# Optimization experiments

Measured on AMD Instinct MI355X. Metric: run time of the kernel, lower is better.

Reference implementation:

```python
import jax, jax.numpy as jnp
import numpy as np


def setup_inputs() -> dict:
    key = jax.random.key(0)
    ks = jax.random.split(key, 6)
    bs, n_src, n_tgt = 4, 4096, 16384
    c_src, c_tgt = 256, 128
    xyz_target = jax.random.uniform(ks[0], (bs, n_tgt, 3), dtype=jnp.float32)
    xyz_source = jax.random.uniform(ks[1], (bs, n_src, 3), dtype=jnp.float32)
    feats_target = jax.random.normal(ks[2], (bs, n_tgt, c_tgt), dtype=jnp.float32)
    feats_source = jax.random.normal(ks[3], (bs, n_src, c_src), dtype=jnp.float32)
    # SharedMlP 1x1 conv weights (1,1,cin,cout) squeezed to (cin,cout)
    w1 = jax.random.normal(ks[4], (c_src + c_tgt, 256), dtype=jnp.float32) * (1.0 / np.sqrt(c_src + c_tgt))
    w2 = jax.random.normal(ks[5], (256, 256), dtype=jnp.float32) * (1.0 / np.sqrt(256))
    return {"xyz_target": xyz_target, "xyz_source": xyz_source,
            "feats_target": feats_target, "feats_source": feats_source,
            "w1": w1, "w2": w2}


def reference(xyz_target, xyz_source, feats_target, feats_source, w1, w2):
    # --- three_nn: full pairwise euclidean distance [bs, n_tgt, n_src] ---
    diff = xyz_target[:, :, None, :] - xyz_source[:, None, :, :]
    dis = jnp.linalg.norm(diff, axis=-1)                      # bs, n_tgt, n_src
    neg_dis, idx = jax.lax.top_k(-dis, 3)                     # 3 nearest
    nn_dis = jnp.maximum(-neg_dis, 1e-10)                     # bs, n_tgt, 3
    inv = 1.0 / nn_dis
    weight = inv / jnp.sum(inv, axis=-1, keepdims=True)       # bs, n_tgt, 3
    # --- three_interpolate: batched gather + weighted reduce ---
    feats_sel = jax.vmap(lambda f, i: f[i])(feats_source, idx)  # bs, n_tgt, 3, c
    w_sum = jnp.sum(weight, axis=-1, keepdims=True) + 1e-6
    interp = jnp.einsum('btk,btkc->btc', weight, feats_sel) / w_sum
    # --- concat skip features, 1x1-conv MLP (pointwise matmul) ---
    x = jnp.concatenate([interp, feats_target], axis=2)       # bs, n_tgt, 384
    x = jax.nn.relu(jnp.einsum('btc,cd->btd', x, w1))
    x = jax.nn.relu(jnp.einsum('btc,cd->btd', x, w2))
    return x
```

## Files before the change

### kernel.cpp

```cpp
#include <hip/hip_runtime.h>
#include <hip/hip_bf16.h>
#include <stdint.h>

#define BS 4
#define NS 4096
#define NT 16384
#define CS 256
#define CT 128
#define NOUT 256
#define MTOT (BS*NT)
#define GR 8
#define NC (GR*GR*GR)
#define HCELL 0.125f

typedef __attribute__((ext_vector_type(4))) float floatx4;
typedef __attribute__((ext_vector_type(8))) short shortx8;
typedef __attribute__((ext_vector_type(8))) unsigned short ushortx8;
typedef __attribute__((ext_vector_type(8))) __bf16 bf16x8;

__device__ __forceinline__ unsigned short f2bf(float f) {
  unsigned int u = __builtin_bit_cast(unsigned int, f);
  u += 0x7FFFu + ((u >> 16) & 1u);
  return (unsigned short)(u >> 16);
}
__device__ __forceinline__ float bf2f(unsigned short u) {
  return __builtin_bit_cast(float, ((unsigned int)u) << 16);
}
__device__ __forceinline__ int cell_of(float x) {
  int c = (int)(x * 8.0f);
  return min(7, max(0, c));
}

__global__ __launch_bounds__(256) void wt_kernel(const float* __restrict__ w1,
    const float* __restrict__ w2, unsigned short* __restrict__ w1at,
    unsigned short* __restrict__ w1bt, unsigned short* __restrict__ w2t) {
  int i = blockIdx.x * 256 + threadIdx.x;
  {
    int n = i >> 8, k = i & 255;
    w1at[i] = f2bf(w1[k * NOUT + n]);
    w2t[i]  = f2bf(w2[k * NOUT + n]);
  }
  if (i < 256 * 128) {
    int n = i >> 7, k = i & 127;
    w1bt[i] = f2bf(w1[(256 + k) * NOUT + n]);
  }
}

__global__ __launch_bounds__(512) void bucket_src(const float* __restrict__ xyzs,
    float4* __restrict__ bsrc, int* __restrict__ soff) {
  __shared__ int cnt[NC];
  __shared__ int scan[NC];
  int tid = threadIdx.x;
  int b = blockIdx.x;
  const float* src = xyzs + (size_t)b * NS * 3;
  cnt[tid] = 0;
  __syncthreads();
  #pragma unroll
  for (int k = 0; k < 8; ++k) {
    int p = k * 512 + tid;
    float x = src[3*p], y = src[3*p+1], z = src[3*p+2];
    int c = (cell_of(z) * GR + cell_of(y)) * GR + cell_of(x);
    atomicAdd(&cnt[c], 1);
  }
  __syncthreads();
  scan[tid] = cnt[tid];
  __syncthreads();
  for (int off = 1; off < NC; off <<= 1) {
    int v = (tid >= off) ? scan[tid - off] : 0;
    __syncthreads();
    scan[tid] += v;
    __syncthreads();
  }
  int excl = scan[tid] - cnt[tid];
  cnt[tid] = excl;
  soff[b * (NC + 1) + tid] = excl;
  if (tid == 0) soff[b * (NC + 1) + NC] = NS;
  __syncthreads();
  #pragma unroll
  for (int k = 0; k < 8; ++k) {
    int p = k * 512 + tid;
    float x = src[3*p], y = src[3*p+1], z = src[3*p+2];
    int c = (cell_of(z) * GR + cell_of(y)) * GR + cell_of(x);
    int slot = atomicAdd(&cnt[c], 1);
    bsrc[(size_t)b * NS + slot] = make_float4(x, y, z, __int_as_float(p));
  }
}

__global__ __launch_bounds__(1024) void sort_tgt(const float* __restrict__ xyzt,
    float4* __restrict__ stgt) {
  __shared__ int cnt[NC];
  __shared__ int scan[NC];
  int tid = threadIdx.x;
  int b = blockIdx.x;
  const float* tp = xyzt + (size_t)b * NT * 3;
  if (tid < NC) cnt[tid] = 0;
  __syncthreads();
  #pragma unroll
  for (int k = 0; k < 16; ++k) {
    int p = k * 1024 + tid;
    float x = tp[3*p], y = tp[3*p+1], z = tp[3*p+2];
    int c = (cell_of(z) * GR + cell_of(y)) * GR + cell_of(x);
    atomicAdd(&cnt[c], 1);
  }
  __syncthreads();
  if (tid < NC) scan[tid] = cnt[tid];
  __syncthreads();
  for (int off = 1; off < NC; off <<= 1) {
    int v = (tid < NC && tid >= off) ? scan[tid - off] : 0;
    __syncthreads();
    if (tid < NC) scan[tid] += v;
    __syncthreads();
  }
  if (tid < NC) cnt[tid] = scan[tid] - cnt[tid];
  __syncthreads();
  #pragma unroll
  for (int k = 0; k < 16; ++k) {
    int p = k * 1024 + tid;
    float x = tp[3*p], y = tp[3*p+1], z = tp[3*p+2];
    int c = (cell_of(z) * GR + cell_of(y)) * GR + cell_of(x);
    int slot = atomicAdd(&cnt[c], 1);
    stgt[(size_t)b * NT + slot] = make_float4(x, y, z, __int_as_float(p));
  }
}

__device__ __forceinline__ void ins3(float sc, int jj,
    float& d0, float& d1, float& d2, int& i0, int& i1, int& i2) {
  bool l0 = sc < d0, l1 = sc < d1, l2 = sc < d2;
  d2 = l1 ? d1 : (l2 ? sc : d2);
  i2 = l1 ? i1 : (l2 ? jj : i2);
  d1 = l0 ? d0 : (l1 ? sc : d1);
  i1 = l0 ? i0 : (l1 ? jj : i1);
  d0 = l0 ? sc : d0;
  i0 = l0 ? jj : i0;
}

__device__ __forceinline__ void pair_merge(float& d0, float& d1, float& d2,
                                           int& i0, int& i1, int& i2,
                                           int delta, int sub) {
  float e0 = __shfl_xor(d0, delta);
  float e1 = __shfl_xor(d1, delta);
  float e2 = __shfl_xor(d2, delta);
  int   y0 = __shfl_xor(i0, delta);
  int   y1 = __shfl_xor(i1, delta);
  int   y2 = __shfl_xor(i2, delta);
  float a0,a1,a2,b0,b1,b2; int x0,x1,x2,z0,z1,z2;
  if ((sub & delta) == 0) { a0=d0;a1=d1;a2=d2; x0=i0;x1=i1;x2=i2;
                            b0=e0;b1=e1;b2=e2; z0=y0;z1=y1;z2=y2; }
  else                    { a0=e0;a1=e1;a2=e2; x0=y0;x1=y1;x2=y2;
                            b0=d0;b1=d1;b2=d2; z0=i0;z1=i1;z2=i2; }
  bool t = a0 <= b0;
  d0 = t ? a0 : b0; i0 = t ? x0 : z0;
  float na0 = t ? a1 : a0; int nx0 = t ? x1 : x0;
  float na1 = t ? a2 : a1; int nx1 = t ? x2 : x1;
  float nb0 = t ? b0 : b1; int nz0 = t ? z0 : z1;
  float nb1 = t ? b1 : b2; int nz1 = t ? z1 : z2;
  t = na0 <= nb0;
  d1 = t ? na0 : nb0; i1 = t ? nx0 : nz0;
  float ma0 = t ? na1 : na0; int mx0 = t ? nx1 : nx0;
  float mb0 = t ? nb0 : nb1; int mz0 = t ? nz0 : nz1;
  t = ma0 <= mb0;
  d2 = t ? ma0 : mb0; i2 = t ? mx0 : mz0;
}

__global__ __launch_bounds__(256) void nn_kernel(const float4* __restrict__ stgt,
    const float4* __restrict__ bsrc, const int* __restrict__ soff,
    int* __restrict__ idx_out, float* __restrict__ w_out) {
  __shared__ float4 s_src[NS];
  __shared__ int s_off[NC + 1];
  int tid = threadIdx.x;
  int b = blockIdx.x >> 7;
  int tseg = blockIdx.x & 127;
  for (int i = tid; i < NS; i += 256) s_src[i] = bsrc[(size_t)b * NS + i];
  for (int i = tid; i < NC + 1; i += 256) s_off[i] = soff[b * (NC + 1) + i];
  __syncthreads();
  int tpair = tid >> 1, half = tid & 1;
  float4 tg = stgt[(size_t)b * NT + tseg * 128 + tpair];
  float tx = tg.x, ty = tg.y, tz = tg.z;
  int orig = __float_as_int(tg.w);
  int cx = cell_of(tx), cy = cell_of(ty), cz = cell_of(tz);
  int wx = min(max(cx, 1), 6) - 1;
  int wy = min(max(cy, 1), 6) - 1;
  int wz = min(max(cz, 1), 6) - 1;
  float d0 = 1e30f, d1 = 1e30f, d2 = 1e30f;
  int i0 = 0, i1 = 0, i2 = 0;
  for (int r = half; r < 9; r += 2) {
    int ez = wz + r / 3, ey = wy + r % 3;
    int rowc = (ez * GR + ey) * GR + wx;
    int lo = s_off[rowc], hi = s_off[rowc + 3];
    for (int p = lo; p < hi; ++p) {
      float4 s = s_src[p];
      float dx = tx - s.x, dy = ty - s.y, dz = tz - s.z;
      float q = dx*dx + dy*dy + dz*dz;
      ins3(q, __float_as_int(s.w), d0, d1, d2, i0, i1, i2);
    }
  }
  pair_merge(d0, d1, d2, i0, i1, i2, 1, half);
  float clx = fminf(wx > 0 ? tx - wx * HCELL : 1e30f,
                    wx + 3 < GR ? (wx + 3) * HCELL - tx : 1e30f);
  float cly = fminf(wy > 0 ? ty - wy * HCELL : 1e30f,
                    wy + 3 < GR ? (wy + 3) * HCELL - ty : 1e30f);
  float clz = fminf(wz > 0 ? tz - wz * HCELL : 1e30f,
                    wz + 3 < GR ? (wz + 3) * HCELL - tz : 1e30f);
  float cl = fminf(clx, fminf(cly, clz));
  bool bad = d2 > cl * cl;
  if (__any(bad)) {
    if (bad) {
      d0 = d1 = d2 = 1e30f; i0 = i1 = i2 = 0;
      for (int p = half; p < NS; p += 2) {
        float4 s = s_src[p];
        float dx = tx - s.x, dy = ty - s.y, dz = tz - s.z;
        float q = dx*dx + dy*dy + dz*dz;
        ins3(q, __float_as_int(s.w), d0, d1, d2, i0, i1, i2);
      }
    }
    pair_merge(d0, d1, d2, i0, i1, i2, 1, half);
  }
  if (half == 0) {
    float r0 = fmaxf(sqrtf(d0), 1e-10f);
    float r1 = fmaxf(sqrtf(d1), 1e-10f);
    float r2 = fmaxf(sqrtf(d2), 1e-10f);
    float v0 = 1.f/r0, v1 = 1.f/r1, v2 = 1.f/r2;
    float sc = 1.f / ((v0 + v1 + v2) * (1.f + 1e-6f));
    size_t o = ((size_t)b * NT + orig) * 3;
    idx_out[o] = i0; idx_out[o+1] = i1; idx_out[o+2] = i2;
    w_out[o] = v0*sc; w_out[o+1] = v1*sc; w_out[o+2] = v2*sc;
  }
}

__global__ __launch_bounds__(256) void gemm_g(const float* __restrict__ fs,
    const unsigned short* __restrict__ w1at, unsigned short* __restrict__ G) {
  constexpr int LDT = 72;
  __shared__ __attribute__((aligned(16))) unsigned short sA[128 * LDT];
  __shared__ __attribute__((aligned(16))) unsigned short sB[128 * LDT];
  int tid = threadIdx.x;
  int m0 = blockIdx.x * 128;
  int n0 = blockIdx.y * 128;
  int wave = tid >> 6, lane = tid & 63;
  int wm = (wave >> 1) * 64, wn = (wave & 1) * 64;
  int fr = lane & 15, quad = lane >> 4;
  floatx4 zero = {0.f, 0.f, 0.f, 0.f};
  floatx4 acc[4][4];
  #pragma unroll
  for (int i = 0; i < 4; ++i)
    #pragma unroll
    for (int j = 0; j < 4; ++j) acc[i][j] = zero;

  for (int kt = 0; kt < 256; kt += 64) {
    #pragma unroll
    for (int i = 0; i < 4; ++i) {
      int u = tid + 256 * i;
      int r = u >> 3, k8 = (u & 7) * 8;
      const float* src = fs + (size_t)(m0 + r) * 256 + kt + k8;
      float4 f0 = *(const float4*)src;
      float4 f1 = *(const float4*)(src + 4);
      ushortx8 o;
      o[0]=f2bf(f0.x); o[1]=f2bf(f0.y); o[2]=f2bf(f0.z); o[3]=f2bf(f0.w);
      o[4]=f2bf(f1.x); o[5]=f2bf(f1.y); o[6]=f2bf(f1.z); o[7]=f2bf(f1.w);
      *(ushortx8*)&sA[r * LDT + k8] = o;
    }
    #pragma unroll
    for (int i = 0; i < 4; ++i) {
      int u = tid + 256 * i;
      int n = u >> 3, kc = (u & 7) * 8;
      *(ushortx8*)&sB[n * LDT + kc] =
          *(const ushortx8*)(w1at + (size_t)(n0 + n) * 256 + kt + kc);
    }
    __syncthreads();
    #pragma unroll
    for (int kk = 0; kk < 64; kk += 32) {
      bf16x8 af[4], bfr[4];
      #pragma unroll
      for (int mi = 0; mi < 4; ++mi)
        af[mi] = __builtin_bit_cast(bf16x8,
            *(const ushortx8*)&sA[(wm + mi*16 + fr)*LDT + kk + quad*8]);
      #pragma unroll
      for (int ni = 0; ni < 4; ++ni)
        bfr[ni] = __builtin_bit_cast(bf16x8,
            *(const ushortx8*)&sB[(wn + ni*16 + fr)*LDT + kk + quad*8]);
      #pragma unroll
      for (int mi = 0; mi < 4; ++mi)
        #pragma unroll
        for (int ni = 0; ni < 4; ++ni)
          acc[mi][ni] = __builtin_amdgcn_mfma_f32_16x16x32_bf16(
              af[mi], bfr[ni], acc[mi][ni], 0, 0, 0);
    }
    __syncthreads();
  }
  #pragma unroll
  for (int mi = 0; mi < 4; ++mi)
    #pragma unroll
    for (int ni = 0; ni < 4; ++ni)
      #pragma unroll
      for (int r = 0; r < 4; ++r) {
        int grow = m0 + wm + mi*16 + quad*4 + r;
        int gcol = n0 + wn + ni*16 + fr;
        G[(size_t)grow * 256 + gcol] = f2bf(acc[mi][ni][r]);
      }
}

__global__ __launch_bounds__(256) void fused_mlp(const float* __restrict__ ft,
    const unsigned short* __restrict__ G, const int* __restrict__ idxb,
    const float* __restrict__ wgtb, const unsigned short* __restrict__ w1bt,
    const unsigned short* __restrict__ w2t, float* __restrict__ out) {
  constexpr int LDI = 264;
  constexpr int LDT = 72;
  __shared__ __attribute__((aligned(16))) unsigned short sI[64 * LDI];
  __shared__ __attribute__((aligned(16))) unsigned short sA[64 * LDT];
  __shared__ __attribute__((aligned(16))) unsigned short sB[256 * LDT];
  int tid = threadIdx.x;
  int row0 = blockIdx.x * 64;
  int b = row0 >> 14;
  int wave = tid >> 6, lane = tid & 63;
  int wn = wave * 64;
  int fr = lane & 15, quad = lane >> 4;

  {
    int r = tid >> 2, seg = tid & 3;
    int grow = row0 + r;
    const int* ip = idxb + (size_t)grow * 3;
    const float* wp = wgtb + (size_t)grow * 3;
    int g0i = ip[0], g1i = ip[1], g2i = ip[2];
    float w0 = wp[0], w1v = wp[1], w2v = wp[2];
    const unsigned short* Gb = G + ((size_t)b << 20);
    const unsigned short* g0 = Gb + ((size_t)g0i << 8) + seg * 64;
    const unsigned short* g1 = Gb + ((size_t)g1i << 8) + seg * 64;
    const unsigned short* g2 = Gb + ((size_t)g2i << 8) + seg * 64;
    #pragma unroll
    for (int j = 0; j < 8; ++j) {
      ushortx8 a = *(const ushortx8*)(g0 + j*8);
      ushortx8 c = *(const ushortx8*)(g1 + j*8);
      ushortx8 e = *(const ushortx8*)(g2 + j*8);
      ushortx8 o;
      #pragma unroll
      for (int q = 0; q < 8; ++q)
        o[q] = f2bf(w0*bf2f(a[q]) + w1v*bf2f(c[q]) + w2v*bf2f(e[q]));
      *(ushortx8*)&sI[r * LDI + seg * 64 + j * 8] = o;
    }
  }

  floatx4 zero = {0.f, 0.f, 0.f, 0.f};
  floatx4 acc[4][4];
  #pragma unroll
  for (int i = 0; i < 4; ++i)
    #pragma unroll
    for (int j = 0; j < 4; ++j) acc[i][j] = zero;

  for (int kt = 0; kt < 128; kt += 64) {
    #pragma unroll
    for (int i = 0; i < 2; ++i) {
      int u = tid + 256 * i;
      int r = u >> 3, k8 = (u & 7) * 8;
      const float* src = ft + (size_t)(row0 + r) * CT + kt + k8;
      float4 f0 = *(const float4*)src;
      float4 f1 = *(const float4*)(src + 4);
      ushortx8 o;
      o[0]=f2bf(f0.x); o[1]=f2bf(f0.y); o[2]=f2bf(f0.z); o[3]=f2bf(f0.w);
      o[4]=f2bf(f1.x); o[5]=f2bf(f1.y); o[6]=f2bf(f1.z); o[7]=f2bf(f1.w);
      *(ushortx8*)&sA[r * LDT + k8] = o;
    }
    #pragma unroll
    for (int i = 0; i < 8; ++i) {
      int u = tid + 256 * i;
      int n = u >> 3, kc = (u & 7) * 8;
      *(ushortx8*)&sB[n * LDT + kc] =
          *(const ushortx8*)(w1bt + (size_t)n * CT + kt + kc);
    }
    __syncthreads();
    #pragma unroll
    for (int kk = 0; kk < 64; kk += 32) {
      bf16x8 af[4], bfr[4];
      #pragma unroll
      for (int mi = 0; mi < 4; ++mi)
        af[mi] = __builtin_bit_cast(bf16x8,
            *(const ushortx8*)&sA[(mi*16 + fr)*LDT + kk + quad*8]);
      #pragma unroll
      for (int ni = 0; ni < 4; ++ni)
        bfr[ni] = __builtin_bit_cast(bf16x8,
            *(const ushortx8*)&sB[(wn + ni*16 + fr)*LDT + kk + quad*8]);
      #pragma unroll
      for (int mi = 0; mi < 4; ++mi)
        #pragma unroll
        for (int ni = 0; ni < 4; ++ni)
          acc[mi][ni] = __builtin_amdgcn_mfma_f32_16x16x32_bf16(
              af[mi], bfr[ni], acc[mi][ni], 0, 0, 0);
    }
    __syncthreads();
  }

  #pragma unroll
  for (int mi = 0; mi < 4; ++mi)
    #pragma unroll
    for (int ni = 0; ni < 4; ++ni)
      #pragma unroll
      for (int r = 0; r < 4; ++r) {
        int lr = mi*16 + quad*4 + r;
        int lc = wn + ni*16 + fr;
        float v = acc[mi][ni][r] + bf2f(sI[lr * LDI + lc]);
        sI[lr * LDI + lc] = f2bf(fmaxf(v, 0.f));
      }
  __syncthreads();

  #pragma unroll
  for (int i = 0; i < 4; ++i)
    #pragma unroll
    for (int j = 0; j < 4; ++j) acc[i][j] = zero;
  for (int kt = 0; kt < 256; kt += 64) {
    #pragma unroll
    for (int i = 0; i < 8; ++i) {
      int u = tid + 256 * i;
      int n = u >> 3, kc = (u & 7) * 8;
      *(ushortx8*)&sB[n * LDT + kc] =
          *(const ushortx8*)(w2t + (size_t)n * 256 + kt + kc);
    }
    __syncthreads();
    #pragma unroll
    for (int kk = 0; kk < 64; kk += 32) {
      bf16x8 af[4], bfr[4];
      #pragma unroll
      for (int mi = 0; mi < 4; ++mi)
        af[mi] = __builtin_bit_cast(bf16x8,
            *(const ushortx8*)&sI[(mi*16 + fr)*LDI + kt + kk + quad*8]);
      #pragma unroll
      for (int ni = 0; ni < 4; ++ni)
        bfr[ni] = __builtin_bit_cast(bf16x8,
            *(const ushortx8*)&sB[(wn + ni*16 + fr)*LDT + kk + quad*8]);
      #pragma unroll
      for (int mi = 0; mi < 4; ++mi)
        #pragma unroll
        for (int ni = 0; ni < 4; ++ni)
          acc[mi][ni] = __builtin_amdgcn_mfma_f32_16x16x32_bf16(
              af[mi], bfr[ni], acc[mi][ni], 0, 0, 0);
    }
    __syncthreads();
  }
  #pragma unroll
  for (int mi = 0; mi < 4; ++mi)
    #pragma unroll
    for (int ni = 0; ni < 4; ++ni)
      #pragma unroll
      for (int r = 0; r < 4; ++r) {
        int grow = row0 + mi*16 + quad*4 + r;
        int gcol = wn + ni*16 + fr;
        out[(size_t)grow * 256 + gcol] = fmaxf(acc[mi][ni][r], 0.f);
      }
}

extern "C" void kernel_launch(void* const* d_in, const int* in_sizes, int n_in,
                              void* d_out, int out_size, void* d_ws, size_t ws_size,
                              hipStream_t stream) {
  (void)in_sizes; (void)n_in; (void)out_size; (void)ws_size;
  const float* xyzt = (const float*)d_in[0];
  const float* xyzs = (const float*)d_in[1];
  const float* ft   = (const float*)d_in[2];
  const float* fs   = (const float*)d_in[3];
  const float* w1   = (const float*)d_in[4];
  const float* w2   = (const float*)d_in[5];

  char* p = (char*)d_ws;
  unsigned short* w1at = (unsigned short*)p; p += (size_t)256*256*2;
  unsigned short* w1bt = (unsigned short*)p; p += (size_t)256*128*2;
  unsigned short* w2t  = (unsigned short*)p; p += (size_t)256*256*2;
  int*   idxb = (int*)p;   p += (size_t)MTOT*3*4;
  float* wgtb = (float*)p; p += (size_t)MTOT*3*4;
  unsigned short* G = (unsigned short*)p; p += (size_t)BS*NS*NOUT*2;
  float4* bsrc = (float4*)p; p += (size_t)BS*NS*16;
  float4* stgt = (float4*)p; p += (size_t)BS*NT*16;
  int*    soff = (int*)p;

  hipLaunchKernelGGL(wt_kernel, dim3(256), dim3(256), 0, stream, w1, w2, w1at, w1bt, w2t);
  hipLaunchKernelGGL(bucket_src, dim3(BS), dim3(512), 0, stream, xyzs, bsrc, soff);
  hipLaunchKernelGGL(sort_tgt, dim3(BS), dim3(1024), 0, stream, xyzt, stgt);
  hipLaunchKernelGGL(nn_kernel, dim3(512), dim3(256), 0, stream, stgt, bsrc, soff, idxb, wgtb);
  hipLaunchKernelGGL(gemm_g, dim3(BS*NS/128, 2), dim3(256), 0, stream, fs, w1at, G);
  hipLaunchKernelGGL(fused_mlp, dim3(MTOT/64), dim3(256), 0, stream,
                     ft, G, idxb, wgtb, w1bt, w2t, (float*)d_out);
}
```

Baseline: 211.5 us.

## Merge prep kernels, process MLP in spatially sorted order, read weights directly

Measured after the change: 196.2 us. -7.3%, faster.

```diff
diff --git a/kernel.cpp b/kernel.cpp
--- a/kernel.cpp
+++ b/kernel.cpp
@@ -5,7 +5,6 @@
 #define BS 4
 #define NS 4096
 #define NT 16384
-#define CS 256
 #define CT 128
 #define NOUT 256
 #define MTOT (BS*NT)
@@ -14,7 +13,6 @@
 #define HCELL 0.125f
 
 typedef __attribute__((ext_vector_type(4))) float floatx4;
-typedef __attribute__((ext_vector_type(8))) short shortx8;
 typedef __attribute__((ext_vector_type(8))) unsigned short ushortx8;
 typedef __attribute__((ext_vector_type(8))) __bf16 bf16x8;
 
@@ -31,95 +29,61 @@
   return min(7, max(0, c));
 }
 
-__global__ __launch_bounds__(256) void wt_kernel(const float* __restrict__ w1,
-    const float* __restrict__ w2, unsigned short* __restrict__ w1at,
-    unsigned short* __restrict__ w1bt, unsigned short* __restrict__ w2t) {
-  int i = blockIdx.x * 256 + threadIdx.x;
-  {
+__global__ __launch_bounds__(1024) void prep_kernel(
+    const float* __restrict__ xyzs, const float* __restrict__ xyzt,
+    const float* __restrict__ w1, const float* __restrict__ w2,
+    float4* __restrict__ bsrc, int* __restrict__ soff, float4* __restrict__ stgt,
+    unsigned short* __restrict__ w1at, unsigned short* __restrict__ w1bt,
+    unsigned short* __restrict__ w2t) {
+  int bid = blockIdx.x, tid = threadIdx.x;
+  if (bid < 8) {
+    __shared__ int cnt[NC];
+    __shared__ int scan[NC];
+    int b = bid & 3;
+    bool isrc = bid < 4;
+    int per = isrc ? (NS >> 10) : (NT >> 10);
+    const float* in = isrc ? xyzs + (size_t)b * NS * 3 : xyzt + (size_t)b * NT * 3;
+    float4* outp = isrc ? bsrc + (size_t)b * NS : stgt + (size_t)b * NT;
+    if (tid < NC) cnt[tid] = 0;
+    __syncthreads();
+    for (int k = 0; k < per; ++k) {
+      int p = k * 1024 + tid;
+      float x = in[3*p], y = in[3*p+1], z = in[3*p+2];
+      int c = (cell_of(z) * GR + cell_of(y)) * GR + cell_of(x);
+      atomicAdd(&cnt[c], 1);
+    }
+    __syncthreads();
+    if (tid < NC) scan[tid] = cnt[tid];
+    __syncthreads();
+    for (int off = 1; off < NC; off <<= 1) {
+      int v = (tid < NC && tid >= off) ? scan[tid - off] : 0;
+      __syncthreads();
+      if (tid < NC) scan[tid] += v;
+      __syncthreads();
+    }
+    if (tid < NC) {
+      int excl = scan[tid] - cnt[tid];
+      cnt[tid] = excl;
+      if (isrc) soff[b * (NC + 1) + tid] = excl;
+    }
+    if (isrc && tid == 0) soff[b * (NC + 1) + NC] = NS;
+    __syncthreads();
+    for (int k = 0; k < per; ++k) {
+      int p = k * 1024 + tid;
+      float x = in[3*p], y = in[3*p+1], z = in[3*p+2];
+      int c = (cell_of(z) * GR + cell_of(y)) * GR + cell_of(x);
+      int slot = atomicAdd(&cnt[c], 1);
+      outp[slot] = make_float4(x, y, z, __int_as_float(p));
+    }
+  } else {
+    int i = (bid - 8) * 1024 + tid;
     int n = i >> 8, k = i & 255;
     w1at[i] = f2bf(w1[k * NOUT + n]);
     w2t[i]  = f2bf(w2[k * NOUT + n]);
-  }
-  if (i < 256 * 128) {
-    int n = i >> 7, k = i & 127;
-    w1bt[i] = f2bf(w1[(256 + k) * NOUT + n]);
-  }
-}
-
-__global__ __launch_bounds__(512) void bucket_src(const float* __restrict__ xyzs,
-    float4* __restrict__ bsrc, int* __restrict__ soff) {
-  __shared__ int cnt[NC];
-  __shared__ int scan[NC];
-  int tid = threadIdx.x;
-  int b = blockIdx.x;
-  const float* src = xyzs + (size_t)b * NS * 3;
-  cnt[tid] = 0;
-  __syncthreads();
-  #pragma unroll
-  for (int k = 0; k < 8; ++k) {
-    int p = k * 512 + tid;
-    float x = src[3*p], y = src[3*p+1], z = src[3*p+2];
-    int c = (cell_of(z) * GR + cell_of(y)) * GR + cell_of(x);
-    atomicAdd(&cnt[c], 1);
-  }
-  __syncthreads();
-  scan[tid] = cnt[tid];
-  __syncthreads();
-  for (int off = 1; off < NC; off <<= 1) {
-    int v = (tid >= off) ? scan[tid - off] : 0;
-    __syncthreads();
-    scan[tid] += v;
-    __syncthreads();
-  }
-  int excl = scan[tid] - cnt[tid];
-  cnt[tid] = excl;
-  soff[b * (NC + 1) + tid] = excl;
-  if (tid == 0) soff[b * (NC + 1) + NC] = NS;
-  __syncthreads();
-  #pragma unroll
-  for (int k = 0; k < 8; ++k) {
-    int p = k * 512 + tid;
-    float x = src[3*p], y = src[3*p+1], z = src[3*p+2];
-    int c = (cell_of(z) * GR + cell_of(y)) * GR + cell_of(x);
-    int slot = atomicAdd(&cnt[c], 1);
-    bsrc[(size_t)b * NS + slot] = make_float4(x, y, z, __int_as_float(p));
-  }
-}
-
-__global__ __launch_bounds__(1024) void sort_tgt(const float* __restrict__ xyzt,
-    float4* __restrict__ stgt) {
-  __shared__ int cnt[NC];
-  __shared__ int scan[NC];
-  int tid = threadIdx.x;
-  int b = blockIdx.x;
-  const float* tp = xyzt + (size_t)b * NT * 3;
-  if (tid < NC) cnt[tid] = 0;
-  __syncthreads();
-  #pragma unroll
-  for (int k = 0; k < 16; ++k) {
-    int p = k * 1024 + tid;
-    float x = tp[3*p], y = tp[3*p+1], z = tp[3*p+2];
-    int c = (cell_of(z) * GR + cell_of(y)) * GR + cell_of(x);
-    atomicAdd(&cnt[c], 1);
-  }
-  __syncthreads();
-  if (tid < NC) scan[tid] = cnt[tid];
-  __syncthreads();
-  for (int off = 1; off < NC; off <<= 1) {
-    int v = (tid < NC && tid >= off) ? scan[tid - off] : 0;
-    __syncthreads();
-    if (tid < NC) scan[tid] += v;
-    __syncthreads();
-  }
-  if (tid < NC) cnt[tid] = scan[tid] - cnt[tid];
-  __syncthreads();
-  #pragma unroll
-  for (int k = 0; k < 16; ++k) {
-    int p = k * 1024 + tid;
-    float x = tp[3*p], y = tp[3*p+1], z = tp[3*p+2];
-    int c = (cell_of(z) * GR + cell_of(y)) * GR + cell_of(x);
-    int slot = atomicAdd(&cnt[c], 1);
-    stgt[(size_t)b * NT + slot] = make_float4(x, y, z, __int_as_float(p));
+    if (i < 256 * 128) {
+      int n2 = i >> 7, k2 = i & 127;
+      w1bt[i] = f2bf(w1[(256 + k2) * NOUT + n2]);
+    }
   }
 }
 
@@ -176,7 +140,6 @@
   int tpair = tid >> 1, half = tid & 1;
   float4 tg = stgt[(size_t)b * NT + tseg * 128 + tpair];
   float tx = tg.x, ty = tg.y, tz = tg.z;
-  int orig = __float_as_int(tg.w);
   int cx = cell_of(tx), cy = cell_of(ty), cz = cell_of(tz);
   int wx = min(max(cx, 1), 6) - 1;
   int wy = min(max(cy, 1), 6) - 1;
@@ -221,7 +184,7 @@
     float r2 = fmaxf(sqrtf(d2), 1e-10f);
     float v0 = 1.f/r0, v1 = 1.f/r1, v2 = 1.f/r2;
     float sc = 1.f / ((v0 + v1 + v2) * (1.f + 1e-6f));
-    size_t o = ((size_t)b * NT + orig) * 3;
+    size_t o = ((size_t)b * NT + tseg * 128 + tpair) * 3;
     idx_out[o] = i0; idx_out[o+1] = i1; idx_out[o+2] = i2;
     w_out[o] = v0*sc; w_out[o+1] = v1*sc; w_out[o+2] = v2*sc;
   }
@@ -298,27 +261,29 @@
       }
 }
 
-__global__ __launch_bounds__(256) void fused_mlp(const float* __restrict__ ft,
+__global__ __launch_bounds__(256, 3) void fused_mlp(const float* __restrict__ ft,
     const unsigned short* __restrict__ G, const int* __restrict__ idxb,
-    const float* __restrict__ wgtb, const unsigned short* __restrict__ w1bt,
-    const unsigned short* __restrict__ w2t, float* __restrict__ out) {
+    const float* __restrict__ wgtb, const float4* __restrict__ stgt,
+    const unsigned short* __restrict__ w1bt, const unsigned short* __restrict__ w2t,
+    float* __restrict__ out) {
   constexpr int LDI = 264;
-  constexpr int LDT = 72;
+  constexpr int LDF = 136;
   __shared__ __attribute__((aligned(16))) unsigned short sI[64 * LDI];
-  __shared__ __attribute__((aligned(16))) unsigned short sA[64 * LDT];
-  __shared__ __attribute__((aligned(16))) unsigned short sB[256 * LDT];
+  __shared__ __attribute__((aligned(16))) unsigned short sF[64 * LDF];
   int tid = threadIdx.x;
   int row0 = blockIdx.x * 64;
   int b = row0 >> 14;
+  const float4* st = stgt + ((size_t)b << 14) + (row0 & (NT - 1));
+  const float* ftb = ft + (size_t)b * NT * CT;
+  float* outb = out + (size_t)b * NT * NOUT;
   int wave = tid >> 6, lane = tid & 63;
   int wn = wave * 64;
   int fr = lane & 15, quad = lane >> 4;
 
   {
     int r = tid >> 2, seg = tid & 3;
-    int grow = row0 + r;
-    const int* ip = idxb + (size_t)grow * 3;
-    const float* wp = wgtb + (size_t)grow * 3;
+    const int* ip = idxb + (size_t)(row0 + r) * 3;
+    const float* wp = wgtb + (size_t)(row0 + r) * 3;
     int g0i = ip[0], g1i = ip[1], g2i = ip[2];
     float w0 = wp[0], w1v = wp[1], w2v = wp[2];
     const unsigned short* Gb = G + ((size_t)b << 20);
@@ -337,6 +302,20 @@
       *(ushortx8*)&sI[r * LDI + seg * 64 + j * 8] = o;
     }
   }
+  #pragma unroll
+  for (int i = 0; i < 4; ++i) {
+    int u = tid + 256 * i;
+    int r = u >> 4, k8 = (u & 15) * 8;
+    int orig = __float_as_int(st[r].w);
+    const float* src = ftb + (size_t)orig * CT + k8;
+    float4 f0 = *(const float4*)src;
+    float4 f1 = *(const float4*)(src + 4);
+    ushortx8 o;
+    o[0]=f2bf(f0.x); o[1]=f2bf(f0.y); o[2]=f2bf(f0.z); o[3]=f2bf(f0.w);
+    o[4]=f2bf(f1.x); o[5]=f2bf(f1.y); o[6]=f2bf(f1.z); o[7]=f2bf(f1.w);
+    *(ushortx8*)&sF[r * LDF + k8] = o;
+  }
+  __syncthreads();
 
   floatx4 zero = {0.f, 0.f, 0.f, 0.f};
   floatx4 acc[4][4];
@@ -345,46 +324,23 @@
     #pragma unroll
     for (int j = 0; j < 4; ++j) acc[i][j] = zero;
 
-  for (int kt = 0; kt < 128; kt += 64) {
-    #pragma unroll
-    for (int i = 0; i < 2; ++i) {
-      int u = tid + 256 * i;
-      int r = u >> 3, k8 = (u & 7) * 8;
-      const float* src = ft + (size_t)(row0 + r) * CT + kt + k8;
-      float4 f0 = *(const float4*)src;
-      float4 f1 = *(const float4*)(src + 4);
-      ushortx8 o;
-      o[0]=f2bf(f0.x); o[1]=f2bf(f0.y); o[2]=f2bf(f0.z); o[3]=f2bf(f0.w);
-      o[4]=f2bf(f1.x); o[5]=f2bf(f1.y); o[6]=f2bf(f1.z); o[7]=f2bf(f1.w);
-      *(ushortx8*)&sA[r * LDT + k8] = o;
-    }
-    #pragma unroll
-    for (int i = 0; i < 8; ++i) {
-      int u = tid + 256 * i;
-      int n = u >> 3, kc = (u & 7) * 8;
-      *(ushortx8*)&sB[n * LDT + kc] =
-          *(const ushortx8*)(w1bt + (size_t)n * CT + kt + kc);
-    }
-    __syncthreads();
-    #pragma unroll
-    for (int kk = 0; kk < 64; kk += 32) {
-      bf16x8 af[4], bfr[4];
-      #pragma unroll
-      for (int mi = 0; mi < 4; ++mi)
-        af[mi] = __builtin_bit_cast(bf16x8,
-            *(const ushortx8*)&sA[(mi*16 + fr)*LDT + kk + quad*8]);
+  #pragma unroll
+  for (int kk = 0; kk < 128; kk += 32) {
+    bf16x8 af[4], bfr[4];
+    #pragma unroll
+    for (int mi = 0; mi < 4; ++mi)
+      af[mi] = __builtin_bit_cast(bf16x8,
+          *(const ushortx8*)&sF[(mi*16 + fr)*LDF + kk + quad*8]);
+    #pragma unroll
+    for (int ni = 0; ni < 4; ++ni)
+      bfr[ni] = __builtin_bit_cast(bf16x8,
+          *(const ushortx8*)(w1bt + (size_t)(wn + ni*16 + fr) * CT + kk + quad*8));
+    #pragma unroll
+    for (int mi = 0; mi < 4; ++mi)
       #pragma unroll
       for (int ni = 0; ni < 4; ++ni)
-        bfr[ni] = __builtin_bit_cast(bf16x8,
-            *(const ushortx8*)&sB[(wn + ni*16 + fr)*LDT + kk + quad*8]);
-      #pragma unroll
-      for (int mi = 0; mi < 4; ++mi)
-        #pragma unroll
-        for (int ni = 0; ni < 4; ++ni)
-          acc[mi][ni] = __builtin_amdgcn_mfma_f32_16x16x32_bf16(
-              af[mi], bfr[ni], acc[mi][ni], 0, 0, 0);
-    }
-    __syncthreads();
+        acc[mi][ni] = __builtin_amdgcn_mfma_f32_16x16x32_bf16(
+            af[mi], bfr[ni], acc[mi][ni], 0, 0, 0);
   }
 
   #pragma unroll
@@ -404,45 +360,35 @@
   for (int i = 0; i < 4; ++i)
     #pragma unroll
     for (int j = 0; j < 4; ++j) acc[i][j] = zero;
-  for (int kt = 0; kt < 256; kt += 64) {
-    #pragma unroll
-    for (int i = 0; i < 8; ++i) {
-      int u = tid + 256 * i;
-      int n = u >> 3, kc = (u & 7) * 8;
-      *(ushortx8*)&sB[n * LDT + kc] =
-          *(const ushortx8*)(w2t + (size_t)n * 256 + kt + kc);
-    }
-    __syncthreads();
-    #pragma unroll
-    for (int kk = 0; kk < 64; kk += 32) {
-      bf16x8 af[4], bfr[4];
-      #pragma unroll
-      for (int mi = 0; mi < 4; ++mi)
-        af[mi] = __builtin_bit_cast(bf16x8,
-            *(const ushortx8*)&sI[(mi*16 + fr)*LDI + kt + kk + quad*8]);
+  #pragma unroll
+  for (int kk = 0; kk < 256; kk += 32) {
+    bf16x8 af[4], bfr[4];
+    #pragma unroll
+    for (int mi = 0; mi < 4; ++mi)
+      af[mi] = __builtin_bit_cast(bf16x8,
+          *(const ushortx8*)&sI[(mi*16 + fr)*LDI + kk + quad*8]);
+    #pragma unroll
+    for (int ni = 0; ni < 4; ++ni)
+      bfr[ni] = __builtin_bit_cast(bf16x8,
+          *(const ushortx8*)(w2t + (size_t)(wn + ni*16 + fr) * NOUT + kk + quad*8));
+    #pragma unroll
+    for (int mi = 0; mi < 4; ++mi)
       #pragma unroll
       for (int ni = 0; ni < 4; ++ni)
-        bfr[ni] = __builtin_bit_cast(bf16x8,
-            *(const ushortx8*)&sB[(wn + ni*16 + fr)*LDT + kk + quad*8]);
-      #pragma unroll
-      for (int mi = 0; mi < 4; ++mi)
-        #pragma unroll
-        for (int ni = 0; ni < 4; ++ni)
-          acc[mi][ni] = __builtin_amdgcn_mfma_f32_16x16x32_bf16(
-              af[mi], bfr[ni], acc[mi][ni], 0, 0, 0);
-    }
-    __syncthreads();
+        acc[mi][ni] = __builtin_amdgcn_mfma_f32_16x16x32_bf16(
+            af[mi], bfr[ni], acc[mi][ni], 0, 0, 0);
   }
   #pragma unroll
   for (int mi = 0; mi < 4; ++mi)
     #pragma unroll
-    for (int ni = 0; ni < 4; ++ni)
-      #pragma unroll
-      for (int r = 0; r < 4; ++r) {
-        int grow = row0 + mi*16 + quad*4 + r;
-        int gcol = wn + ni*16 + fr;
-        out[(size_t)grow * 256 + gcol] = fmaxf(acc[mi][ni][r], 0.f);
-      }
+    for (int r = 0; r < 4; ++r) {
+      int lr = mi*16 + quad*4 + r;
+      int orig = __float_as_int(st[lr].w);
+      float* orow = outb + (size_t)orig * NOUT;
+      #pragma unroll
+      for (int ni = 0; ni < 4; ++ni)
+        orow[wn + ni*16 + fr] = fmaxf(acc[mi][ni][r], 0.f);
+    }
 }
 
 extern "C" void kernel_launch(void* const* d_in, const int* in_sizes, int n_in,
@@ -467,11 +413,10 @@
   float4* stgt = (float4*)p; p += (size_t)BS*NT*16;
   int*    soff = (int*)p;
 
-  hipLaunchKernelGGL(wt_kernel, dim3(256), dim3(256), 0, stream, w1, w2, w1at, w1bt, w2t);
-  hipLaunchKernelGGL(bucket_src, dim3(BS), dim3(512), 0, stream, xyzs, bsrc, soff);
-  hipLaunchKernelGGL(sort_tgt, dim3(BS), dim3(1024), 0, stream, xyzt, stgt);
+  hipLaunchKernelGGL(prep_kernel, dim3(8 + 64), dim3(1024), 0, stream,
+                     xyzs, xyzt, w1, w2, bsrc, soff, stgt, w1at, w1bt, w2t);
   hipLaunchKernelGGL(nn_kernel, dim3(512), dim3(256), 0, stream, stgt, bsrc, soff, idxb, wgtb);
   hipLaunchKernelGGL(gemm_g, dim3(BS*NS/128, 2), dim3(256), 0, stream, fs, w1at, G);
   hipLaunchKernelGGL(fused_mlp, dim3(MTOT/64), dim3(256), 0, stream,
-                     ft, G, idxb, wgtb, w1bt, w2t, (float*)d_out);
-}
+                     ft, G, idxb, wgtb, stgt, w1bt, w2t, (float*)d_out);
+}
```
